# Kernel optimization log

Measured on AMD Instinct MI355X. Metric: run time of the kernel, lower is better.

The kernel has to match this reference:

```python
import jax, jax.numpy as jnp
import numpy as np
from math import log2

FPS = 100.0
MIN_BPM = 55.0
MAX_BPM = 215.0
NUM_TEMPI = 60
NUM_BEATS = 4
TRANS_LAMBDA = 100.0
OBS_LAMBDA = 16.0
NUM_FRAMES = 6000


def _intervals():
    mi = 60.0 * FPS / MAX_BPM
    ma = 60.0 * FPS / MIN_BPM
    iv = np.arange(round(mi), round(ma) + 1)
    if NUM_TEMPI < len(iv):
        n = NUM_TEMPI
        iv = np.zeros(0)
        while len(iv) < NUM_TEMPI:
            iv = np.unique(np.round(np.logspace(log2(mi), log2(ma), n, base=2)))
            n += 1
    return iv.astype(np.int64)


def _state_space():
    iv = _intervals()                      # (I,) tempo intervals in frames
    nsb = int(iv.sum())                    # states per beat
    first = np.concatenate([[0], np.cumsum(iv)[:-1]]).astype(np.int64)
    last = (np.cumsum(iv) - 1).astype(np.int64)
    pos_b = np.concatenate([np.arange(i) / float(i) for i in iv])
    positions = np.concatenate([pos_b + b for b in range(NUM_BEATS)])  # (S,)
    first_states = np.stack([first + b * nsb for b in range(NUM_BEATS)])  # (B,I)
    last_states = np.stack([last + b * nsb for b in range(NUM_BEATS)])    # (B,I)
    # exponential tempo transition (madmom exponential_transition, norm=True)
    ratio = iv[None, :].astype(np.float64) / iv[:, None].astype(np.float64)
    prob = np.exp(-TRANS_LAMBDA * np.abs(ratio - 1.0))
    prob[prob <= np.spacing(1)] = 0.0
    prob /= prob.sum(axis=1, keepdims=True)
    log_t = np.where(prob > 0, np.log(np.maximum(prob, 1e-300)), -1e30).astype(np.float32)
    log_trans = np.tile(log_t[None], (NUM_BEATS, 1, 1))  # same lambda per beat boundary
    prev_last = np.stack([last_states[(b - 1) % NUM_BEATS] for b in range(NUM_BEATS)])
    # observation pointers: 0 = no beat, 1 = beat, 2 = downbeat
    frac = positions % 1.0
    beat_idx = np.floor(positions).astype(np.int64)
    ptr = np.where(frac < 1.0 / OBS_LAMBDA, np.where(beat_idx == 0, 2, 1), 0)
    return first_states, prev_last, log_trans, ptr, nsb * NUM_BEATS


def setup_inputs() -> dict:
    key = jax.random.key(0)
    first_states, prev_last, log_trans, pointer, S = _state_space()
    # beat/downbeat activation probabilities; scaled so beat+downbeat < 1
    acts = jax.random.uniform(key, (NUM_FRAMES, 2), dtype=jnp.float32) * 0.45
    return {
        "activations": acts,
        "log_trans": jnp.asarray(log_trans),
        "prev_last": jnp.asarray(prev_last, dtype=jnp.int32),
        "first_states": jnp.asarray(first_states, dtype=jnp.int32),
        "pointer": jnp.asarray(pointer, dtype=jnp.int32),
        "num_states": S,
    }


def reference(activations, log_trans, prev_last, first_states, pointer, num_states):
    S = int(num_states)
    NEG = jnp.float32(-1e30)
    a_b = activations[:, 0]
    a_d = activations[:, 1]
    # log observation densities: [no-beat, beat, downbeat], shape (F, 3)
    dens = jnp.stack([
        jnp.log((1.0 - a_b - a_d) / (OBS_LAMBDA - 1.0)),
        jnp.log(a_b),
        jnp.log(a_d),
    ], axis=1)
    first_flat = first_states.reshape(-1)  # (B*I,)
    base_ptr = jnp.arange(S, dtype=jnp.int32) - 1  # default predecessor s-1

    def step(v, dens_t):
        # within-interval advance: state s comes from s-1 with prob 1
        v_shift = jnp.concatenate([jnp.full((1,), NEG, v.dtype), v[:-1]])
        # beat boundaries: first states of beat b from last states of beat b-1
        cand = v[prev_last]                      # (B, I)
        scores = cand[:, :, None] + log_trans    # (B, I_from, I_to)
        best = scores.max(axis=1).reshape(-1)    # (B*I,)
        arg = scores.argmax(axis=1)              # (B, I_to)
        bp_first = jnp.take_along_axis(prev_last, arg.astype(jnp.int32), axis=1).reshape(-1)
        ptr = base_ptr.at[first_flat].set(bp_first)
        v_new = v_shift.at[first_flat].set(best) + dens_t[pointer]
        return v_new, ptr

    v0 = jnp.full((S,), -jnp.log(jnp.float32(S)))  # uniform initial distribution
    v_final, bps = jax.lax.scan(step, v0, dens)    # bps: (F, S) backpointers
    last_state = jnp.argmax(v_final).astype(jnp.int32)
    logp = v_final[last_state]

    def back(s, bp_t):
        p = bp_t[s]
        return p, p

    _, earlier = jax.lax.scan(back, last_state, bps[1:], reverse=True)
    path = jnp.concatenate([earlier, last_state[None]])  # (F,) best state sequence
    return path, logp
```

## Files before the change

### kernel.cpp

```cpp
#include <hip/hip_runtime.h>
#include <stdint.h>


#define NB 4
#define KF 15
#define QW 16
#define NPMAX 256
#define TBATCH 32
#define NEGV -1.0e30f

__device__ __forceinline__ float bf16u_to_f(uint16_t u) {
    union { uint32_t i; float f; } v; v.i = ((uint32_t)u) << 16; return v.f;
}

template<int CTRL>
__device__ __forceinline__ int dpp_i(int x) {
    return __builtin_amdgcn_update_dpp(0, x, CTRL, 0xF, 0xF, true);
}
template<int CTRL>
__device__ __forceinline__ float dpp_f(float x) {
    return __int_as_float(dpp_i<CTRL>(__float_as_int(x)));
}

__device__ __forceinline__ void load_acts(const void* p, int isbf, int t, float& a, float& d) {
    if (isbf) {
        const uint16_t* u = (const uint16_t*)p;
        uint32_t w = *(const uint32_t*)(u + 2 * t);
        a = bf16u_to_f((uint16_t)w); d = bf16u_to_f((uint16_t)(w >> 16));
    } else {
        const float2* f = (const float2*)p;
        float2 v = f[t]; a = v.x; d = v.y;
    }
}

template<bool FAST>
__global__ __launch_bounds__(1024) void dbn_viterbi_kernel(
    const void* __restrict__ acts_raw,
    const void* __restrict__ lt_raw,
    const int*  __restrict__ prev_last,
    const int*  __restrict__ first_states,
    float*      __restrict__ out,
    float*      __restrict__ ws_lastv,
    uint8_t*    __restrict__ ws_argi,
    int T, int S, int F)
{
    const int tid  = (int)threadIdx.x;
    const int NP   = NB * T;
    const int lane = tid & 63;
    const int wvx  = tid >> 6;

    __shared__ alignas(16) float lastv2[2 * NB * 64];
    __shared__ float bestv[NPMAX];
    __shared__ float bound[16];
    __shared__ int   fsld[NPMAX];
    __shared__ int   plds[NPMAX];
    __shared__ int   pref[NPMAX + 1];
    __shared__ float dens_s[4];
    __shared__ float wvs[16];
    __shared__ int   wss[16];
    __shared__ int   flag_s;
    __shared__ uint8_t argi_s[TBATCH * 240 + 16];

    if (tid == 0) {
        const uint16_t* au = (const uint16_t*)acts_raw;
        int bf = 1;
        for (int i = 0; i < 32; i++) {
            uint16_t e = au[2 * i];
            uint8_t h8 = (uint8_t)(e >> 8);
            if (!(e == 0 || (h8 >= 0x20 && h8 < 0x40))) bf = 0;
        }
        flag_s = bf;
    }
    if (tid < NP)          { fsld[tid] = first_states[tid]; plds[tid] = prev_last[tid]; }
    if (tid < 2 * NB * 64) lastv2[tid] = NEGV;
    __syncthreads();
    const int isbf = flag_s;
    const int nsb  = S / NB;
    const uint16_t* lt_u = (const uint16_t*)lt_raw;
    const float*    lt_f = (const float*)lt_raw;

    if (tid == 0) {
        int acc = 0;
        for (int g = 0; g < NP; g++) {
            int b = g / T, ib = g - b * T;
            int end = (ib + 1 < T) ? fsld[g + 1] : (b + 1) * nsb;
            int L = end - fsld[g];
            pref[g] = acc; acc += (L + KF - 1) / KF;
        }
        pref[NP] = acc;
    }
    __syncthreads();
    const int NT = pref[NP];

    const bool act_u = (tid < NT);
    int g_own = 0, startg = 0, Lg = 1, sb = 0, lq = 0;
    bool is_last = false, pv2 = false;
    if (act_u) {
        int lo = 0, hi = NP - 1;
        while (lo < hi) { int mid = (lo + hi + 1) >> 1; if (pref[mid] <= tid) lo = mid; else hi = mid - 1; }
        g_own = lo;
        int j = tid - pref[lo];
        int b = g_own / T, ib = g_own - b * T;
        startg = fsld[g_own];
        int end = (ib + 1 < T) ? fsld[g_own + 1] : (b + 1) * nsb;
        Lg = end - startg;
        int n = (Lg + KF - 1) / KF;
        sb = startg + Lg - KF * (n - j);
        is_last = (j == n - 1);
        lq = (b << 6) + ib;
        pv2 = (b == 0);
    }
    bool hb[KF], hq[KF];
    #pragma unroll
    for (int kk = 0; kk < KF; kk++) {
        int i = sb + kk - startg;
        hq[kk] = act_u && (i <= 0);
        hb[kk] = act_u && (16 * i < Lg);
    }

    const int g_a = tid >> 2, k4 = tid & 3;
    const bool act_g = (g_a < NP);
    float ltreg[QW];
    #pragma unroll
    for (int u = 0; u < QW; u++) ltreg[u] = NEGV;
    int rowbase = 0;
    if (act_g) {
        int b = g_a / T, j = g_a - (g_a / T) * T;
        rowbase = ((b + 3) & 3) << 6;
        #pragma unroll
        for (int u = 0; u < QW; u++) {
            int i = k4 * QW + u;
            if (i < T) {
                int idx = (b * T + i) * T + j;
                ltreg[u] = isbf ? bf16u_to_f(lt_u[idx]) : lt_f[idx];
            }
        }
    }

    const float vinit = -logf((float)S);
    float vreg[KF];
    #pragma unroll
    for (int kk = 0; kk < KF; kk++) vreg[kk] = vinit;
    if (act_u && is_last) lastv2[256 + lq] = vinit;
    if (lane == 63) bound[wvx] = vinit;
    float inc_pipe = vinit;
    float ab_c = 0.0f, ad_c = 0.0f;
    if (wvx == 15 && lane >= 60 && lane < 63) load_acts(acts_raw, isbf, 0, ab_c, ad_c);

    for (int t = 0; t < F; t++) {
        __syncthreads();
        const float* lvR = lastv2 + (((t & 1) ^ 1) << 8);
        float inc_use = inc_pipe;
        if (lane == 0) inc_use = bound[(wvx + 15) & 15];

        if (wvx == 15) {
            if (lane >= 60 && lane < 63) {
                int c3 = lane - 60;
                float dv = (c3 == 0) ? logf(((1.0f - ab_c) - ad_c) / 15.0f)
                         : (c3 == 1) ? logf(ab_c) : logf(ad_c);
                dens_s[c3] = dv;
                if (t + 1 < F) load_acts(acts_raw, isbf, t + 1, ab_c, ad_c);
            }
        } else if (act_g) {
            const float* rowp = &lvR[rowbase + k4 * QW];
            float4 l0 = *(const float4*)(rowp + 0);
            float4 l1 = *(const float4*)(rowp + 4);
            float4 l2 = *(const float4*)(rowp + 8);
            float4 l3 = *(const float4*)(rowp + 12);
            if (FAST) {
                float m0 = fmaxf(fmaxf(l0.x + ltreg[0],  l0.y + ltreg[1]),
                                 fmaxf(l0.z + ltreg[2],  l0.w + ltreg[3]));
                float m1 = fmaxf(fmaxf(l1.x + ltreg[4],  l1.y + ltreg[5]),
                                 fmaxf(l1.z + ltreg[6],  l1.w + ltreg[7]));
                float m2 = fmaxf(fmaxf(l2.x + ltreg[8],  l2.y + ltreg[9]),
                                 fmaxf(l2.z + ltreg[10], l2.w + ltreg[11]));
                float m3 = fmaxf(fmaxf(l3.x + ltreg[12], l3.y + ltreg[13]),
                                 fmaxf(l3.z + ltreg[14], l3.w + ltreg[15]));
                float mv = fmaxf(fmaxf(m0, m1), fmaxf(m2, m3));
                mv = fmaxf(mv, dpp_f<0xB1>(mv));
                mv = fmaxf(mv, dpp_f<0x4E>(mv));
                if (k4 == 0) bestv[g_a] = mv;
            } else {
                float cand[QW] = { l0.x, l0.y, l0.z, l0.w, l1.x, l1.y, l1.z, l1.w,
                                   l2.x, l2.y, l2.z, l2.w, l3.x, l3.y, l3.z, l3.w };
                float mv = -INFINITY; int ai = 0;
                #pragma unroll
                for (int u = 0; u < QW; u++) {
                    float sc = cand[u] + ltreg[u];
                    if (sc > mv) { mv = sc; ai = k4 * QW + u; }
                }
                float ov = dpp_f<0xB1>(mv); int oa = dpp_i<0xB1>(ai);
                if (ov > mv || (ov == mv && oa < ai)) { mv = ov; ai = oa; }
                ov = dpp_f<0x4E>(mv); oa = dpp_i<0x4E>(ai);
                if (ov > mv || (ov == mv && oa < ai)) { mv = ov; ai = oa; }
                if (k4 == 0) {
                    bestv[g_a] = mv;
                    argi_s[(t & (TBATCH - 1)) * NP + g_a] = (uint8_t)ai;
                }
            }
        }

        __syncthreads();
        float d0  = dens_s[0];
        float dpv = pv2 ? dens_s[2] : dens_s[1];
        float bq  = bestv[g_own];
        #pragma unroll
        for (int kk = KF - 1; kk >= 0; kk--) {
            float prev = (kk == 0) ? inc_use : vreg[kk - 1];
            prev = hq[kk] ? bq : prev;
            float add = hb[kk] ? dpv : d0;
            vreg[kk] = prev + add;
        }
        float* lvW = lastv2 + ((t & 1) << 8);
        if (act_u && is_last) lvW[lq] = vreg[KF - 1];
        if (lane == 63) bound[wvx] = vreg[KF - 1];
        inc_pipe = __shfl_up(vreg[KF - 1], 1, 64);

        if (FAST) {
            if (wvx == 15 && t > 0 && lane < (NP >> 2)) {
                int c = lane << 2;
                int bb = c / T, cib = c - bb * T;
                float4 v4 = *(const float4*)&lvR[(bb << 6) + cib];
                *(float4*)&ws_lastv[(size_t)(t - 1) * NP + c] = v4;
            }
        } else {
            int tB = t & (TBATCH - 1);
            if (tB == TBATCH - 1 || t == F - 1) {
                int nbytes = (tB + 1) * NP;
                int t0 = t - tB;
                for (int off = tid * 4; off < nbytes; off += 4096) {
                    uint32_t w = *(const uint32_t*)&argi_s[off];
                    *(uint32_t*)&ws_argi[(size_t)t0 * NP + off] = w;
                }
            }
        }
    }

    __syncthreads();
    float mv = -INFINITY; int ms = 0x7FFFFFFF;
    #pragma unroll
    for (int kk = 0; kk < KF; kk++) {
        int s = sb + kk;
        bool valid = act_u && (s >= startg);
        float v = vreg[kk];
        if (valid && v > mv) { mv = v; ms = s; }
    }
    #pragma unroll
    for (int d = 1; d < 64; d <<= 1) {
        float ov = __shfl_xor(mv, d, 64);
        int   os = __shfl_xor(ms, d, 64);
        if (ov > mv || (ov == mv && os < ms)) { mv = ov; ms = os; }
    }
    if (lane == 0) { wvs[wvx] = mv; wss[wvx] = ms; }
    __syncthreads();

    if (tid == 0) {
        float bm = -INFINITY; int bs = 0x7FFFFFFF;
        for (int w = 0; w < 16; w++) {
            if (wvs[w] > bm || (wvs[w] == bm && wss[w] < bs)) { bm = wvs[w]; bs = wss[w]; }
        }
        int s = bs;
        int t = F - 1;
        out[F - 1] = (float)s;
        while (t > 0) {
            int b = s / nsb;
            int lo = b * T, hi = b * T + T - 1;
            while (lo < hi) { int mid = (lo + hi + 1) >> 1; if (fsld[mid] <= s) lo = mid; else hi = mid - 1; }
            int p = lo;
            int run = s - fsld[p];
            if (run == 0) {
                int ai;
                if (FAST) {
                    int jt = p - b * T;
                    int pb = (b + 3) & 3;
                    const float* lrow = &ws_lastv[(size_t)(t - 1) * NP + pb * T];
                    float bmv = -INFINITY; ai = 0;
                    for (int i = 0; i < T; i++) {
                        int idx = (b * T + i) * T + jt;
                        float ltv = isbf ? bf16u_to_f(lt_u[idx]) : lt_f[idx];
                        float sc = lrow[i] + ltv;
                        if (sc > bmv) { bmv = sc; ai = i; }
                    }
                } else {
                    ai = ws_argi[(size_t)t * NP + p];
                }
                s = plds[b * T + ai];
                out[t - 1] = (float)s;
                t--;
            } else {
                int m = (run < t) ? run : t;
                for (int jj = 0; jj < m; jj++) out[t - 1 - jj] = (float)(s - 1 - jj);
                s -= m; t -= m;
            }
        }
        out[F] = bm;
    }
}

extern "C" void kernel_launch(void* const* d_in, const int* in_sizes, int n_in,
                              void* d_out, int out_size, void* d_ws, size_t ws_size,
                              hipStream_t stream) {
    const int F  = in_sizes[0] / 2;
    const int NP = in_sizes[2];
    const int T  = NP / NB;
    const int S  = in_sizes[4];

    const bool fast = (ws_size >= (size_t)F * NP * 4) && ((T & 3) == 0) && (NP <= NPMAX);

    if (fast) {
        hipLaunchKernelGGL(dbn_viterbi_kernel<true>, dim3(1), dim3(1024), 0, stream,
                           d_in[0], d_in[1],
                           (const int*)d_in[2], (const int*)d_in[3],
                           (float*)d_out, (float*)d_ws, (uint8_t*)d_ws,
                           T, S, F);
    } else {
        hipLaunchKernelGGL(dbn_viterbi_kernel<false>, dim3(1), dim3(1024), 0, stream,
                           d_in[0], d_in[1],
                           (const int*)d_in[2], (const int*)d_in[3],
                           (float*)d_out, (float*)d_ws, (uint8_t*)d_ws,
                           T, S, F);
    }
}
```

Measured before the change: 6.490 ms.

## Add v2 Viterbi kernel with precomputed densities, banded transitions and ring-buffered boundary values

Adds a new single-block kernel that precomputes log observation densities into workspace, keeps the tempo-transition column in registers and exploits band sparsity to cut the per-frame max over previous tempi. Boundary last-state values are kept in a 32-row LDS ring and flushed to global memory in batches by a dedicated wave. The backtrace recomputes the argmax from the stored values rather than using stored argmax indices. This aims to shorten the serial per-frame critical path. The cost is more LDS, an extra workspace region, and a slower backtrace that recomputes each transition.

```diff
diff --git a/kernel.cpp b/kernel.cpp
--- a/kernel.cpp
+++ b/kernel.cpp
@@ -33,15 +33,306 @@
     }
 }
 
-template<bool FAST>
-__global__ __launch_bounds__(1024) void dbn_viterbi_kernel(
+__global__ __launch_bounds__(1024) void dbn_viterbi_v2(
     const void* __restrict__ acts_raw,
     const void* __restrict__ lt_raw,
     const int*  __restrict__ prev_last,
     const int*  __restrict__ first_states,
     float*      __restrict__ out,
     float*      __restrict__ ws_lastv,
-    uint8_t*    __restrict__ ws_argi,
+    float*      __restrict__ ws_dens,
+    int T, int S, int F)
+{
+    const int tid  = (int)threadIdx.x;
+    const int NP   = NB * T;
+    const int lane = tid & 63;
+    const int wvx  = tid >> 6;
+
+    __shared__ alignas(16) float lring[32 * 256];
+    __shared__ alignas(16) float densr[64 * 4];
+    __shared__ float bestv[NPMAX];
+    __shared__ float bound[16];
+    __shared__ int   fsld[NPMAX];
+    __shared__ int   plds[NPMAX];
+    __shared__ int   pref[NPMAX + 1];
+    __shared__ float wvs[16];
+    __shared__ int   wss[16];
+    __shared__ int   flag_s, mspan_s;
+
+    if (tid == 0) {
+        const uint16_t* au = (const uint16_t*)acts_raw;
+        int bf = 1;
+        for (int i = 0; i < 32; i++) {
+            uint16_t e = au[2 * i];
+            uint8_t h8 = (uint8_t)(e >> 8);
+            if (!(e == 0 || (h8 >= 0x20 && h8 < 0x40))) bf = 0;
+        }
+        flag_s = bf; mspan_s = 0;
+    }
+    if (tid < NP) { fsld[tid] = first_states[tid]; plds[tid] = prev_last[tid]; }
+    for (int i = tid; i < 32 * 256; i += 1024) lring[i] = NEGV;
+    __syncthreads();
+    const int isbf = flag_s;
+    const int nsb  = S / NB;
+    const uint16_t* lt_u = (const uint16_t*)lt_raw;
+    const float*    lt_f = (const float*)lt_raw;
+
+    for (int f = tid; f < F; f += 1024) {
+        float ab, ad;
+        load_acts(acts_raw, isbf, f, ab, ad);
+        float4 r;
+        r.x = logf(((1.0f - ab) - ad) / 15.0f);
+        r.y = logf(ab);
+        r.z = logf(ad);
+        r.w = 0.0f;
+        *(float4*)&ws_dens[f * 4] = r;
+    }
+    __threadfence();
+
+    if (tid == 0) {
+        int acc = 0;
+        for (int g = 0; g < NP; g++) {
+            int b = g / T, ib = g - b * T;
+            int end = (ib + 1 < T) ? fsld[g + 1] : (b + 1) * nsb;
+            int L = end - fsld[g];
+            pref[g] = acc; acc += (L + KF - 1) / KF;
+        }
+        pref[NP] = acc;
+    }
+    __syncthreads();
+    const int NT = pref[NP];
+
+    const bool act_u = (tid < NT);
+    int g_own = 0, startg = 0, Lg = 1, sb = 0, lq = 0;
+    bool is_last = false, pv2 = false;
+    if (act_u) {
+        int lo = 0, hi = NP - 1;
+        while (lo < hi) { int mid = (lo + hi + 1) >> 1; if (pref[mid] <= tid) lo = mid; else hi = mid - 1; }
+        g_own = lo;
+        int j = tid - pref[lo];
+        int b = g_own / T, ib = g_own - b * T;
+        startg = fsld[g_own];
+        int end = (ib + 1 < T) ? fsld[g_own + 1] : (b + 1) * nsb;
+        Lg = end - startg;
+        int n = (Lg + KF - 1) / KF;
+        sb = startg + Lg - KF * (n - j);
+        is_last = (j == n - 1);
+        lq = (b << 6) + ib;
+        pv2 = (b == 0);
+    }
+    bool hb[KF], hq[KF];
+    #pragma unroll
+    for (int kk = 0; kk < KF; kk++) {
+        int i = sb + kk - startg;
+        hq[kk] = act_u && (i <= 0);
+        hb[kk] = act_u && (16 * i < Lg);
+    }
+
+    const int g_a = tid >> 2, k4 = tid & 3;
+    const bool act_g = (g_a < NP);
+    int rowbase = 0, lo_b = 0;
+    int b_a = 0, j_a = 0;
+    if (act_g) {
+        b_a = g_a / T; j_a = g_a - b_a * T;
+        rowbase = ((b_a + 3) & 3) << 6;
+        int lo = T, hi = 0;
+        for (int i = 0; i < T; i++) {
+            int idx = (b_a * T + i) * T + j_a;
+            float v = isbf ? bf16u_to_f(lt_u[idx]) : lt_f[idx];
+            if (v > -1e29f) { if (i < lo) lo = i; hi = i; }
+        }
+        lo_b = lo;
+        if (k4 == 0) atomicMax(&mspan_s, hi - lo + 1);
+    }
+    __syncthreads();
+    const bool banded = (mspan_s <= 44);
+    float ltreg[QW];
+    #pragma unroll
+    for (int u = 0; u < QW; u++) ltreg[u] = NEGV;
+    int cb = 0;
+    if (act_g) {
+        if (banded) {
+            cb = (lo_b & ~3) + 12 * k4;
+            if (cb > 52) cb = 52;
+        } else {
+            cb = 16 * k4;
+        }
+        const int nu = banded ? 12 : 16;
+        for (int u = 0; u < nu; u++) {
+            int i = cb + u;
+            if (i < T) {
+                int idx = (b_a * T + i) * T + j_a;
+                ltreg[u] = isbf ? bf16u_to_f(lt_u[idx]) : lt_f[idx];
+            }
+        }
+    }
+
+    const float vinit = -logf((float)S);
+    float vreg[KF];
+    #pragma unroll
+    for (int kk = 0; kk < KF; kk++) vreg[kk] = vinit;
+    if (act_u && is_last) lring[(31 << 8) + lq] = vinit;
+    if (lane == 63) bound[wvx] = vinit;
+    float inc_pipe = vinit;
+    if (tid < 64 && tid < F) {
+        float4 r = *(const float4*)&ws_dens[tid * 4];
+        *(float4*)&densr[tid * 4] = r;
+    }
+
+    const int WQ = NP >> 2;
+    const int TQ = T >> 2;
+
+    for (int t = 0; t < F; t++) {
+        __syncthreads();
+        const float* lvR = &lring[((t + 31) & 31) << 8];
+        float inc_use = inc_pipe;
+        if (lane == 0) inc_use = bound[(wvx + 15) & 15];
+
+        if (wvx == 15) {
+            if ((t & 31) == 0 && t >= 32 && lane < 32) {
+                int fr = t + 32 + lane;
+                if (fr < F) {
+                    float4 r = *(const float4*)&ws_dens[fr * 4];
+                    *(float4*)&densr[(fr & 63) * 4] = r;
+                }
+            }
+            if ((t & 15) == 0 && t > 0 && lane < WQ) {
+                int c = lane;
+                int beat = c / TQ;
+                int srcoff = 4 * c + 4 * beat;
+                int t0 = t - 16;
+                for (int r2 = 0; r2 < 16; r2++) {
+                    int row = t0 + r2;
+                    float4 v4 = *(const float4*)&lring[((row & 31) << 8) + srcoff];
+                    *(float4*)&ws_lastv[(size_t)row * NP + 4 * c] = v4;
+                }
+            }
+        } else if (act_g) {
+            const float* rowp = lvR + rowbase + cb;
+            if (banded) {
+                float4 l0 = *(const float4*)(rowp + 0);
+                float4 l1 = *(const float4*)(rowp + 4);
+                float4 l2 = *(const float4*)(rowp + 8);
+                float m0 = fmaxf(fmaxf(l0.x + ltreg[0], l0.y + ltreg[1]),
+                                 fmaxf(l0.z + ltreg[2], l0.w + ltreg[3]));
+                float m1 = fmaxf(fmaxf(l1.x + ltreg[4], l1.y + ltreg[5]),
+                                 fmaxf(l1.z + ltreg[6], l1.w + ltreg[7]));
+                float m2 = fmaxf(fmaxf(l2.x + ltreg[8], l2.y + ltreg[9]),
+                                 fmaxf(l2.z + ltreg[10], l2.w + ltreg[11]));
+                float mv = fmaxf(fmaxf(m0, m1), m2);
+                mv = fmaxf(mv, dpp_f<0xB1>(mv));
+                mv = fmaxf(mv, dpp_f<0x4E>(mv));
+                if (k4 == 0) bestv[g_a] = mv;
+            } else {
+                float4 l0 = *(const float4*)(rowp + 0);
+                float4 l1 = *(const float4*)(rowp + 4);
+                float4 l2 = *(const float4*)(rowp + 8);
+                float4 l3 = *(const float4*)(rowp + 12);
+                float m0 = fmaxf(fmaxf(l0.x + ltreg[0], l0.y + ltreg[1]),
+                                 fmaxf(l0.z + ltreg[2], l0.w + ltreg[3]));
+                float m1 = fmaxf(fmaxf(l1.x + ltreg[4], l1.y + ltreg[5]),
+                                 fmaxf(l1.z + ltreg[6], l1.w + ltreg[7]));
+                float m2 = fmaxf(fmaxf(l2.x + ltreg[8], l2.y + ltreg[9]),
+                                 fmaxf(l2.z + ltreg[10], l2.w + ltreg[11]));
+                float m3 = fmaxf(fmaxf(l3.x + ltreg[12], l3.y + ltreg[13]),
+                                 fmaxf(l3.z + ltreg[14], l3.w + ltreg[15]));
+                float mv = fmaxf(fmaxf(m0, m1), fmaxf(m2, m3));
+                mv = fmaxf(mv, dpp_f<0xB1>(mv));
+                mv = fmaxf(mv, dpp_f<0x4E>(mv));
+                if (k4 == 0) bestv[g_a] = mv;
+            }
+        }
+
+        __syncthreads();
+        int doff = (t & 63) << 2;
+        float d0  = densr[doff];
+        float dpv = densr[doff + (pv2 ? 2 : 1)];
+        float bq  = bestv[g_own];
+        #pragma unroll
+        for (int kk = KF - 1; kk >= 0; kk--) {
+            float prev = (kk == 0) ? inc_use : vreg[kk - 1];
+            prev = hq[kk] ? bq : prev;
+            float add = hb[kk] ? dpv : d0;
+            vreg[kk] = prev + add;
+        }
+        if (act_u && is_last) lring[((t & 31) << 8) + lq] = vreg[KF - 1];
+        if (lane == 63) bound[wvx] = vreg[KF - 1];
+        inc_pipe = __shfl_up(vreg[KF - 1], 1, 64);
+    }
+
+    __syncthreads();
+    if (wvx == 15 && lane < WQ) {
+        int lastf = (F - 1) & ~15;
+        int c = lane;
+        int beat = c / TQ;
+        int srcoff = 4 * c + 4 * beat;
+        for (int row = lastf; row <= F - 2; row++) {
+            float4 v4 = *(const float4*)&lring[((row & 31) << 8) + srcoff];
+            *(float4*)&ws_lastv[(size_t)row * NP + 4 * c] = v4;
+        }
+        __threadfence();
+    }
+
+    float mv = -INFINITY; int ms = 0x7FFFFFFF;
+    #pragma unroll
+    for (int kk = 0; kk < KF; kk++) {
+        int s = sb + kk;
+        bool valid = act_u && (s >= startg);
+        float v = vreg[kk];
+        if (valid && v > mv) { mv = v; ms = s; }
+    }
+    #pragma unroll
+    for (int d = 1; d < 64; d <<= 1) {
+        float ov = __shfl_xor(mv, d, 64);
+        int   os = __shfl_xor(ms, d, 64);
+        if (ov > mv || (ov == mv && os < ms)) { mv = ov; ms = os; }
+    }
+    if (lane == 0) { wvs[wvx] = mv; wss[wvx] = ms; }
+    __syncthreads();
+
+    if (tid == 0) {
+        float bm = -INFINITY; int bs = 0x7FFFFFFF;
+        for (int w = 0; w < 16; w++) {
+            if (wvs[w] > bm || (wvs[w] == bm && wss[w] < bs)) { bm = wvs[w]; bs = wss[w]; }
+        }
+        int s = bs;
+        int t = F - 1;
+        out[F - 1] = (float)s;
+        while (t > 0) {
+            int b = s / nsb;
+            int lo = b * T, hi = b * T + T - 1;
+            while (lo < hi) { int mid = (lo + hi + 1) >> 1; if (fsld[mid] <= s) lo = mid; else hi = mid - 1; }
+            int p = lo;
+            int run = s - fsld[p];
+            if (run == 0) {
+                int jt = p - b * T;
+                int pb = (b + 3) & 3;
+                const float* lrow = &ws_lastv[(size_t)(t - 1) * NP + pb * T];
+                float bmv = -INFINITY; int ai = 0;
+                for (int i = 0; i < T; i++) {
+                    int idx = (b * T + i) * T + jt;
+                    float ltv = isbf ? bf16u_to_f(lt_u[idx]) : lt_f[idx];
+                    float sc = lrow[i] + ltv;
+                    if (sc > bmv) { bmv = sc; ai = i; }
+                }
+                s = plds[b * T + ai];
+                out[t - 1] = (float)s;
+                t--;
+            } else {
+                int m = (run < t) ? run : t;
+                for (int jj = 0; jj < m; jj++) out[t - 1 - jj] = (float)(s - 1 - jj);
+                s -= m; t -= m;
+            }
+        }
+        out[F] = bm;
+    }
+}
+
+template<bool FAST>
+__global__ __launch_bounds__(1024) void dbn_viterbi_kernel(
+    const void* __restrict__ acts_raw, const void* __restrict__ lt_raw,
+    const int* __restrict__ prev_last, const int* __restrict__ first_states,
+    float* __restrict__ out, float* __restrict__ ws_lastv, uint8_t* __restrict__ ws_argi,
     int T, int S, int F)
 {
     const int tid  = (int)threadIdx.x;
@@ -305,19 +596,27 @@
     const int T  = NP / NB;
     const int S  = in_sizes[4];
 
-    const bool fast = (ws_size >= (size_t)F * NP * 4) && ((T & 3) == 0) && (NP <= NPMAX);
-
-    if (fast) {
+    const size_t need2 = ((size_t)F * NP + 4 * (size_t)F) * 4;
+    const bool okgeom = ((T & 3) == 0) && (NP <= NPMAX) && (T <= 64) && (F >= 2);
+    const bool fast2  = okgeom && (ws_size >= need2);
+    const bool fast1  = okgeom && (ws_size >= (size_t)F * NP * 4);
+
+    if (fast2) {
+        float* ws_lv = (float*)d_ws;
+        float* ws_de = ws_lv + (size_t)F * NP;
+        hipLaunchKernelGGL(dbn_viterbi_v2, dim3(1), dim3(1024), 0, stream,
+                           d_in[0], d_in[1],
+                           (const int*)d_in[2], (const int*)d_in[3],
+                           (float*)d_out, ws_lv, ws_de, T, S, F);
+    } else if (fast1) {
         hipLaunchKernelGGL(dbn_viterbi_kernel<true>, dim3(1), dim3(1024), 0, stream,
                            d_in[0], d_in[1],
                            (const int*)d_in[2], (const int*)d_in[3],
-                           (float*)d_out, (float*)d_ws, (uint8_t*)d_ws,
-                           T, S, F);
+                           (float*)d_out, (float*)d_ws, (uint8_t*)d_ws, T, S, F);
     } else {
         hipLaunchKernelGGL(dbn_viterbi_kernel<false>, dim3(1), dim3(1024), 0, stream,
                            d_in[0], d_in[1],
                            (const int*)d_in[2], (const int*)d_in[3],
-                           (float*)d_out, (float*)d_ws, (uint8_t*)d_ws,
-                           T, S, F);
+                           (float*)d_out, (float*)d_ws, (uint8_t*)d_ws, T, S, F);
     }
 }
```

Result: faster. 6.212 ms (-4.3%).
